# Optimization experiments

Measured on AMD Instinct MI355X. Metric: run time of the kernel, lower is better.

The kernel has to match this reference:

```python
import jax, jax.numpy as jnp
import numpy as np

B, C_IN, L = 4, 512, 16384
C_RED = C_IN // 2  # q/k/v reduced channels = 256
BL = 64            # sliding-window block size
NEG = -jnp.inf


def setup_inputs() -> dict:
    key = jax.random.key(0)
    ks = jax.random.split(key, 8)
    x1 = jax.random.normal(ks[0], (B, C_IN, L), dtype=jnp.float32)
    x2 = jax.random.normal(ks[1], (B, C_IN, L), dtype=jnp.float32)
    mask = jnp.ones((B, 1, L), dtype=jnp.float32)
    s = 0.02
    Wq = jax.random.normal(ks[2], (C_RED, C_IN), dtype=jnp.float32) * s
    Wk = jax.random.normal(ks[3], (C_RED, C_IN), dtype=jnp.float32) * s
    Wv = jax.random.normal(ks[4], (C_RED, C_IN), dtype=jnp.float32) * s
    Wo = jax.random.normal(ks[5], (C_IN, C_RED), dtype=jnp.float32) * s
    bq = jnp.zeros((C_RED,), jnp.float32)
    bk = jnp.zeros((C_RED,), jnp.float32)
    bv = jnp.zeros((C_RED,), jnp.float32)
    bo = jnp.zeros((C_IN,), jnp.float32)
    return {"x1": x1, "x2": x2, "mask": mask, "Wq": Wq, "bq": bq,
            "Wk": Wk, "bk": bk, "Wv": Wv, "bv": bv, "Wo": Wo, "bo": bo}


def _conv1x1(W, b, x):
    # x: (B, Cin, L) -> (B, Cout, L)
    return jnp.einsum('oc,bcl->bol', W, x) + b[None, :, None]


def reference(x1, x2, mask, Wq, bq, Wk, bk, Wv, bv, Wo, bo):
    # encoder stage: value comes from x1 (x2 unused)
    q = _conv1x1(Wq, bq, x1)  # (B, C, L)
    k = _conv1x1(Wk, bk, x1)
    v = _conv1x1(Wv, bv, x1)

    Bq, C, Lq = q.shape
    bl = BL
    nb = (Lq + bl - 1) // bl
    pad = nb * bl - Lq
    if pad > 0:
        q = jnp.pad(q, ((0, 0), (0, 0), (0, pad)))
        k = jnp.pad(k, ((0, 0), (0, 0), (0, pad)))
        v = jnp.pad(v, ((0, 0), (0, 0), (0, pad)))
        mask = jnp.pad(mask, ((0, 0), (0, 0), (0, pad)))

    # non-overlapping windows: (B, C, nb, bl)
    qb = q.reshape(Bq, C, nb, bl)
    kb = k.reshape(Bq, C, nb, bl)
    vb = v.reshape(Bq, C, nb, bl)
    mb = mask.reshape(Bq, 1, nb, bl)  # (B,1,nb,bl)

    scale = 1.0 / jnp.sqrt(jnp.float32(C))
    # per-block attention scores: (B, nb, bl_i, bl_j)
    scores = jnp.einsum('bcni,bcnj->bnij', qb, kb) * scale
    key_mask = mb[:, 0, :, None, :]  # (B, nb, 1, bl_j)
    scores = jnp.where(key_mask == 0, NEG, scores)
    probs = jax.nn.softmax(scores, axis=-1)
    attn = jnp.einsum('bnij,bcnj->bcni', probs, vb)  # (B, C, nb, bl)

    h = jax.nn.relu(attn)
    out = jnp.einsum('oc,bcni->boni', Wo, h) + bo[None, :, None, None]
    out = out.reshape(Bq, Wo.shape[0], nb * bl)
    if pad > 0:
        out = out[:, :, :Lq]
    return out
```

## Files before the change

### kernel.cpp

```cpp
#include <hip/hip_runtime.h>
#include <hip/hip_fp16.h>
#include <stdint.h>

#define BB    4
#define CIN   512
#define CRED  256
#define LL    16384
#define NBLK  256
#define WELEM 131072

typedef _Float16 half8 __attribute__((ext_vector_type(8)));
typedef float    f32x4 __attribute__((ext_vector_type(4)));

#define SWZ(r) (((r)&7)<<4)

#define QBASE   524288
#define TILE_E  16384
#define MAT_E   16777216
#define WS_NEED ((size_t)(QBASE + 3 * MAT_E) * 2)

__global__ void convert_weights(const float* __restrict__ Wq,
                                const float* __restrict__ Wk,
                                const float* __restrict__ Wv,
                                const float* __restrict__ Wo,
                                _Float16* __restrict__ dst) {
    int i = blockIdx.x * blockDim.x + threadIdx.x;
    int m = i >> 17;
    int e = i & (WELEM - 1);
    const float* src = (m == 0) ? Wq : (m == 1) ? Wk : (m == 2) ? Wv : Wo;
    dst[(size_t)m * WELEM + e] = (_Float16)src[e];
}

__global__ __launch_bounds__(256, 2)
void qkv_gemm(const float* __restrict__ x1, const _Float16* __restrict__ W,
              const float* __restrict__ bq, const float* __restrict__ bk,
              const float* __restrict__ bv, _Float16* __restrict__ ws) {
    extern __shared__ char lds[];
    const int tid = threadIdx.x;
    const int wid = tid >> 6;
    const int l15 = tid & 15;
    const int l4  = (tid & 63) >> 4;
    const int b   = blockIdx.x >> 8;
    const int n   = blockIdx.x & 255;

    {
        const int jx = tid & 15;
        const int rg = tid >> 4;
        const float* xp = x1 + ((size_t)b * CIN + 8 * rg) * LL + n * 64 + 4 * jx;
        #pragma unroll
        for (int i = 0; i < 4; ++i) {
            f32x4 r[8];
            #pragma unroll
            for (int r8 = 0; r8 < 8; ++r8)
                r[r8] = *(const f32x4*)(xp + (size_t)(128 * i + r8) * LL);
            #pragma unroll
            for (int u = 0; u < 4; ++u) {
                const int j = 4 * jx + u;
                union { _Float16 h[8]; half8 v; } pk;
                #pragma unroll
                for (int r8 = 0; r8 < 8; ++r8) pk.h[r8] = (_Float16)r[r8][u];
                *(half8*)(lds + j * 1024 + ((16 * rg + 256 * i) ^ SWZ(j))) = pk.v;
            }
        }
    }
    __syncthreads();

    const size_t t = (size_t)blockIdx.x * TILE_E;
    #pragma unroll
    for (int p = 0; p < 3; ++p) {
        f32x4 am[4][4];
        #pragma unroll
        for (int m = 0; m < 4; ++m)
            #pragma unroll
            for (int q = 0; q < 4; ++q) am[m][q] = (f32x4){0.f, 0.f, 0.f, 0.f};
        const _Float16* wp = W + (size_t)p * WELEM + (size_t)(wid * 64 + l15) * CIN + l4 * 8;
        #pragma unroll 4
        for (int ks = 0; ks < 16; ++ks) {
            const int kb = ks * 64 + l4 * 16;
            half8 xb[4];
            #pragma unroll
            for (int nt = 0; nt < 4; ++nt) {
                const int j = nt * 16 + l15;
                xb[nt] = *(const half8*)(lds + j * 1024 + (kb ^ SWZ(j)));
            }
            #pragma unroll
            for (int mt = 0; mt < 4; ++mt) {
                half8 wf = *(const half8*)(wp + mt * 16 * CIN + ks * 32);
                #pragma unroll
                for (int nt = 0; nt < 4; ++nt)
                    am[mt][nt] = __builtin_amdgcn_mfma_f32_16x16x32_f16(wf, xb[nt], am[mt][nt], 0, 0, 0);
            }
        }
        const float* bias = (p == 0) ? bq : (p == 1) ? bk : bv;
        if (p < 2) {
            _Float16* dst = ws + QBASE + (size_t)p * MAT_E + t;
            #pragma unroll
            for (int mt = 0; mt < 4; ++mt) {
                const int c0 = wid * 64 + mt * 16 + l4 * 4;
                f32x4 b4 = *(const f32x4*)(bias + c0);
                #pragma unroll
                for (int nt = 0; nt < 4; ++nt) {
                    const int j = nt * 16 + l15;
                    union { _Float16 h[4]; uint64_t q; } pk;
                    #pragma unroll
                    for (int ri = 0; ri < 4; ++ri)
                        pk.h[ri] = (_Float16)(am[mt][nt][ri] + b4[ri]);
                    *(uint64_t*)(dst + (size_t)j * 256 + c0) = pk.q;
                }
            }
        } else {
            _Float16* dst = ws + QBASE + 2 * (size_t)MAT_E + t;
            #pragma unroll
            for (int mt = 0; mt < 4; ++mt) {
                const int c0 = wid * 64 + mt * 16 + l4 * 4;
                f32x4 b4 = *(const f32x4*)(bias + c0);
                #pragma unroll
                for (int nt = 0; nt < 4; ++nt) {
                    const int j = nt * 16 + l15;
                    #pragma unroll
                    for (int ri = 0; ri < 4; ++ri)
                        dst[(size_t)(c0 + ri) * 64 + j] = (_Float16)(am[mt][nt][ri] + b4[ri]);
                }
            }
        }
    }
}

#define BH_OFF 0
#define BP_OFF 32768
#define LDS_B  40960

__global__ __launch_bounds__(256, 3)
void attn_out(const float* __restrict__ mask, const _Float16* __restrict__ ws,
              const float* __restrict__ bo, float* __restrict__ out) {
    extern __shared__ char lds[];
    const int tid = threadIdx.x;
    const int wid = tid >> 6;
    const int l15 = tid & 15;
    const int l4  = (tid & 63) >> 4;
    const int b   = blockIdx.x >> 8;
    const int n   = blockIdx.x & 255;

    const size_t t = (size_t)blockIdx.x * TILE_E;
    const _Float16* qt = ws + QBASE + t;
    const _Float16* kt = qt + MAT_E;
    const _Float16* vt = qt + 2 * (size_t)MAT_E;
    const _Float16* Wo = ws + 3 * (size_t)WELEM;

    {
        const int i0 = wid * 16;
        f32x4 sa[4];
        #pragma unroll
        for (int jt = 0; jt < 4; ++jt) sa[jt] = (f32x4){0.f, 0.f, 0.f, 0.f};
        #pragma unroll
        for (int ks = 0; ks < 8; ++ks) {
            half8 qa = *(const half8*)(qt + (size_t)(i0 + l15) * 256 + ks * 32 + l4 * 8);
            #pragma unroll
            for (int jt = 0; jt < 4; ++jt) {
                half8 kf = *(const half8*)(kt + (size_t)(jt * 16 + l15) * 256 + ks * 32 + l4 * 8);
                sa[jt] = __builtin_amdgcn_mfma_f32_16x16x32_f16(qa, kf, sa[jt], 0, 0, 0);
            }
        }
        float msk[4];
        #pragma unroll
        for (int jt = 0; jt < 4; ++jt)
            msk[jt] = mask[(size_t)b * LL + n * 64 + jt * 16 + l15];
        #pragma unroll
        for (int ri = 0; ri < 4; ++ri) {
            float v[4];
            #pragma unroll
            for (int jt = 0; jt < 4; ++jt)
                v[jt] = (msk[jt] == 0.f) ? -1e30f : sa[jt][ri] * 0.0625f;
            float mx = fmaxf(fmaxf(v[0], v[1]), fmaxf(v[2], v[3]));
            mx = fmaxf(mx, __shfl_xor(mx, 1));
            mx = fmaxf(mx, __shfl_xor(mx, 2));
            mx = fmaxf(mx, __shfl_xor(mx, 4));
            mx = fmaxf(mx, __shfl_xor(mx, 8));
            float e[4], sum = 0.f;
            #pragma unroll
            for (int jt = 0; jt < 4; ++jt) { e[jt] = __expf(v[jt] - mx); sum += e[jt]; }
            sum += __shfl_xor(sum, 1);
            sum += __shfl_xor(sum, 2);
            sum += __shfl_xor(sum, 4);
            sum += __shfl_xor(sum, 8);
            const float inv = 1.f / sum;
            const int i = i0 + l4 * 4 + ri;
            #pragma unroll
            for (int jt = 0; jt < 4; ++jt) {
                const int j = jt * 16 + l15;
                *(_Float16*)(lds + BP_OFF + i * 128 + ((2 * j) ^ SWZ(i))) =
                    (_Float16)(e[jt] * inv);
            }
        }
    }
    __syncthreads();

    {
        const int cb = wid * 64;
        f32x4 pv[4][4];
        #pragma unroll
        for (int m = 0; m < 4; ++m)
            #pragma unroll
            for (int q = 0; q < 4; ++q) pv[m][q] = (f32x4){0.f, 0.f, 0.f, 0.f};
        #pragma unroll
        for (int ks = 0; ks < 2; ++ks) {
            const int kb = ks * 64 + l4 * 16;
            half8 pb[4];
            #pragma unroll
            for (int nt = 0; nt < 4; ++nt) {
                const int i = nt * 16 + l15;
                pb[nt] = *(const half8*)(lds + BP_OFF + i * 128 + (kb ^ SWZ(i)));
            }
            #pragma unroll
            for (int mt = 0; mt < 4; ++mt) {
                half8 va = *(const half8*)(vt + (size_t)(cb + mt * 16 + l15) * 64 + ks * 32 + l4 * 8);
                #pragma unroll
                for (int nt = 0; nt < 4; ++nt)
                    pv[mt][nt] = __builtin_amdgcn_mfma_f32_16x16x32_f16(va, pb[nt], pv[mt][nt], 0, 0, 0);
            }
        }
        #pragma unroll
        for (int mt = 0; mt < 4; ++mt) {
            const int c0 = cb + mt * 16 + l4 * 4;
            #pragma unroll
            for (int nt = 0; nt < 4; ++nt) {
                const int j = nt * 16 + l15;
                union { _Float16 h[4]; uint64_t q; } hp;
                #pragma unroll
                for (int ri = 0; ri < 4; ++ri)
                    hp.h[ri] = (_Float16)fmaxf(pv[mt][nt][ri], 0.f);
                *(uint64_t*)(lds + BH_OFF + j * 512 + ((2 * c0) ^ SWZ(j))) = hp.q;
            }
        }
    }
    __syncthreads();

    #pragma unroll
    for (int op = 0; op < 2; ++op) {
        const int mbo = wid * 128 + op * 64;
        const _Float16* wob = Wo + (size_t)(mbo + l15) * CRED + l4 * 8;
        f32x4 oa[4][4];
        #pragma unroll
        for (int m = 0; m < 4; ++m)
            #pragma unroll
            for (int q = 0; q < 4; ++q) oa[m][q] = (f32x4){0.f, 0.f, 0.f, 0.f};
        #pragma unroll 4
        for (int ks = 0; ks < 8; ++ks) {
            const int kb = ks * 64 + l4 * 16;
            half8 hb[4];
            #pragma unroll
            for (int nt = 0; nt < 4; ++nt) {
                const int i = nt * 16 + l15;
                hb[nt] = *(const half8*)(lds + BH_OFF + i * 512 + (kb ^ SWZ(i)));
            }
            #pragma unroll
            for (int mt = 0; mt < 4; ++mt) {
                half8 wa = *(const half8*)(wob + mt * 16 * CRED + ks * 32);
                #pragma unroll
                for (int nt = 0; nt < 4; ++nt)
                    oa[mt][nt] = __builtin_amdgcn_mfma_f32_16x16x32_f16(wa, hb[nt], oa[mt][nt], 0, 0, 0);
            }
        }
        #pragma unroll
        for (int mt = 0; mt < 4; ++mt) {
            const int o0 = mbo + mt * 16 + l4 * 4;
            f32x4 bov = *(const f32x4*)(bo + o0);
            #pragma unroll
            for (int ri = 0; ri < 4; ++ri) {
                float* orow = out + ((size_t)b * CIN + (o0 + ri)) * LL + n * 64;
                #pragma unroll
                for (int nt = 0; nt < 4; ++nt)
                    orow[nt * 16 + l15] = oa[mt][nt][ri] + bov[ri];
            }
        }
    }
}

#define XT_OFF 0
#define Q_OFF  0
#define K_OFF  32768
#define V_OFF  32768
#define H_OFF  0
#define P_OFF  65536
#define MSK_OFF 73728
#define LDS_BYTES 73984

__global__ __launch_bounds__(256, 2)
void att_fused(const float* __restrict__ x1, const float* __restrict__ mask,
               const _Float16* __restrict__ W,
               const float* __restrict__ bq, const float* __restrict__ bk,
               const float* __restrict__ bv, const float* __restrict__ bo,
               float* __restrict__ out) {
    extern __shared__ char lds[];
    const int tid  = threadIdx.x;
    const int wid  = tid >> 6;
    const int lane = tid & 63;
    const int l15  = lane & 15;
    const int l4   = lane >> 4;
    const int blk  = blockIdx.x;
    const int b    = blk >> 8;
    const int n    = blk & 255;

    const _Float16* Wq = W;
    const _Float16* Wk = W + WELEM;
    const _Float16* Wv = W + 2 * WELEM;
    const _Float16* Wo = W + 3 * WELEM;

    {
        const int jx = tid & 15;
        const int rb = tid >> 4;
        const float* xbase = x1 + ((size_t)b * CIN + 2 * rb) * LL + n * 64 + 4 * jx;
        #pragma unroll
        for (int i = 0; i < 16; ++i) {
            f32x4 a = *(const f32x4*)(xbase + (size_t)(32 * i) * LL);
            f32x4 c = *(const f32x4*)(xbase + (size_t)(32 * i + 1) * LL);
            const int col = 4 * rb + 64 * i;
            #pragma unroll
            for (int u = 0; u < 4; ++u) {
                union { _Float16 h[2]; uint32_t w; } p;
                p.h[0] = (_Float16)a[u];
                p.h[1] = (_Float16)c[u];
                const int j = 4 * jx + u;
                *(uint32_t*)(lds + XT_OFF + j * 1024 + (col ^ SWZ(j))) = p.w;
            }
        }
        if (tid < 64)
            *(float*)(lds + MSK_OFF + tid * 4) = mask[(size_t)b * LL + n * 64 + tid];
    }
    __syncthreads();

    uint64_t qh[4][4], kh[4][4], vh[4][4];
    #pragma unroll
    for (int pass = 0; pass < 4; ++pass) {
        f32x4 aQ[4], aK[4], aV[4];
        #pragma unroll
        for (int q = 0; q < 4; ++q) {
            aQ[q] = (f32x4){0.f, 0.f, 0.f, 0.f};
            aK[q] = (f32x4){0.f, 0.f, 0.f, 0.f};
            aV[q] = (f32x4){0.f, 0.f, 0.f, 0.f};
        }
        const int mrow = wid * 64 + pass * 16 + l15;
        const _Float16* wqp = Wq + (size_t)mrow * CIN + l4 * 8;
        const _Float16* wkp = Wk + (size_t)mrow * CIN + l4 * 8;
        const _Float16* wvp = Wv + (size_t)mrow * CIN + l4 * 8;
        #pragma unroll 4
        for (int ks = 0; ks < 16; ++ks) {
            const int kb = ks * 64 + l4 * 16;
            half8 xb[4];
            #pragma unroll
            for (int nt = 0; nt < 4; ++nt) {
                const int j = nt * 16 + l15;
                xb[nt] = *(const half8*)(lds + XT_OFF + j * 1024 + (kb ^ SWZ(j)));
            }
            half8 aq = *(const half8*)(wqp + ks * 32);
            half8 ak = *(const half8*)(wkp + ks * 32);
            half8 av = *(const half8*)(wvp + ks * 32);
            #pragma unroll
            for (int nt = 0; nt < 4; ++nt) {
                aQ[nt] = __builtin_amdgcn_mfma_f32_16x16x32_f16(aq, xb[nt], aQ[nt], 0, 0, 0);
                aK[nt] = __builtin_amdgcn_mfma_f32_16x16x32_f16(ak, xb[nt], aK[nt], 0, 0, 0);
                aV[nt] = __builtin_amdgcn_mfma_f32_16x16x32_f16(av, xb[nt], aV[nt], 0, 0, 0);
            }
        }
        const int c0 = wid * 64 + pass * 16 + l4 * 4;
        f32x4 bqv = *(const f32x4*)(bq + c0);
        f32x4 bkv = *(const f32x4*)(bk + c0);
        f32x4 bvv = *(const f32x4*)(bv + c0);
        #pragma unroll
        for (int nt = 0; nt < 4; ++nt) {
            union { _Float16 h[4]; uint64_t q; } qp, kp, vp;
            #pragma unroll
            for (int ri = 0; ri < 4; ++ri) {
                qp.h[ri] = (_Float16)(aQ[nt][ri] + bqv[ri]);
                kp.h[ri] = (_Float16)(aK[nt][ri] + bkv[ri]);
                vp.h[ri] = (_Float16)(aV[nt][ri] + bvv[ri]);
            }
            qh[pass][nt] = qp.q;
            kh[pass][nt] = kp.q;
            vh[pass][nt] = vp.q;
        }
    }
    __syncthreads();

    #pragma unroll
    for (int pass = 0; pass < 4; ++pass) {
        const int c0 = wid * 64 + pass * 16 + l4 * 4;
        #pragma unroll
        for (int nt = 0; nt < 4; ++nt) {
            const int j = nt * 16 + l15;
            *(uint64_t*)(lds + Q_OFF + j * 512 + ((2 * c0) ^ SWZ(j))) = qh[pass][nt];
            *(uint64_t*)(lds + K_OFF + j * 512 + ((2 * c0) ^ SWZ(j))) = kh[pass][nt];
        }
    }
    __syncthreads();

    {
        const int i0 = wid * 16;
        f32x4 sa[4];
        #pragma unroll
        for (int jt = 0; jt < 4; ++jt) sa[jt] = (f32x4){0.f, 0.f, 0.f, 0.f};
        #pragma unroll
        for (int ks = 0; ks < 8; ++ks) {
            const int kb = ks * 64 + l4 * 16;
            const int iq = i0 + l15;
            half8 qa = *(const half8*)(lds + Q_OFF + iq * 512 + (kb ^ SWZ(iq)));
            #pragma unroll
            for (int jt = 0; jt < 4; ++jt) {
                const int jr = jt * 16 + l15;
                half8 kf = *(const half8*)(lds + K_OFF + jr * 512 + (kb ^ SWZ(jr)));
                sa[jt] = __builtin_amdgcn_mfma_f32_16x16x32_f16(qa, kf, sa[jt], 0, 0, 0);
            }
        }
        float msk[4];
        #pragma unroll
        for (int jt = 0; jt < 4; ++jt)
            msk[jt] = *(const float*)(lds + MSK_OFF + (jt * 16 + l15) * 4);
        #pragma unroll
        for (int ri = 0; ri < 4; ++ri) {
            float v[4];
            #pragma unroll
            for (int jt = 0; jt < 4; ++jt)
                v[jt] = (msk[jt] == 0.f) ? -1e30f : sa[jt][ri] * 0.0625f;
            float mx = fmaxf(fmaxf(v[0], v[1]), fmaxf(v[2], v[3]));
            mx = fmaxf(mx, __shfl_xor(mx, 1));
            mx = fmaxf(mx, __shfl_xor(mx, 2));
            mx = fmaxf(mx, __shfl_xor(mx, 4));
            mx = fmaxf(mx, __shfl_xor(mx, 8));
            float e[4], sum = 0.f;
            #pragma unroll
            for (int jt = 0; jt < 4; ++jt) { e[jt] = __expf(v[jt] - mx); sum += e[jt]; }
            sum += __shfl_xor(sum, 1);
            sum += __shfl_xor(sum, 2);
            sum += __shfl_xor(sum, 4);
            sum += __shfl_xor(sum, 8);
            const float inv = 1.f / sum;
            const int i = i0 + l4 * 4 + ri;
            #pragma unroll
            for (int jt = 0; jt < 4; ++jt) {
                const int j = jt * 16 + l15;
                *(_Float16*)(lds + P_OFF + i * 128 + ((2 * j) ^ SWZ(i))) =
                    (_Float16)(e[jt] * inv);
            }
        }
    }
    __syncthreads();

    #pragma unroll
    for (int pass = 0; pass < 4; ++pass) {
        const int c0 = wid * 64 + pass * 16 + l4 * 4;
        #pragma unroll
        for (int nt = 0; nt < 4; ++nt) {
            const int j = nt * 16 + l15;
            const uint64_t v64 = vh[pass][nt];
            #pragma unroll
            for (int ri = 0; ri < 4; ++ri) {
                const int c = c0 + ri;
                *(uint16_t*)(lds + V_OFF + c * 128 + ((2 * j) ^ SWZ(c))) =
                    (uint16_t)(v64 >> (16 * ri));
            }
        }
    }
    __syncthreads();

    {
        const int cb = wid * 64;
        f32x4 pv[4][4];
        #pragma unroll
        for (int m = 0; m < 4; ++m)
            #pragma unroll
            for (int q = 0; q < 4; ++q) pv[m][q] = (f32x4){0.f, 0.f, 0.f, 0.f};
        #pragma unroll
        for (int ks = 0; ks < 2; ++ks) {
            const int kb = ks * 64 + l4 * 16;
            half8 pb[4];
            #pragma unroll
            for (int nt = 0; nt < 4; ++nt) {
                const int i = nt * 16 + l15;
                pb[nt] = *(const half8*)(lds + P_OFF + i * 128 + (kb ^ SWZ(i)));
            }
            #pragma unroll
            for (int mt = 0; mt < 4; ++mt) {
                const int c = cb + mt * 16 + l15;
                half8 va = *(const half8*)(lds + V_OFF + c * 128 + ((kb) ^ SWZ(c)));
                #pragma unroll
                for (int nt = 0; nt < 4; ++nt)
                    pv[mt][nt] = __builtin_amdgcn_mfma_f32_16x16x32_f16(va, pb[nt], pv[mt][nt], 0, 0, 0);
            }
        }
        #pragma unroll
        for (int mt = 0; mt < 4; ++mt) {
            const int c0 = cb + mt * 16 + l4 * 4;
            #pragma unroll
            for (int nt = 0; nt < 4; ++nt) {
                const int j = nt * 16 + l15;
                union { _Float16 h[4]; uint64_t q; } hp;
                #pragma unroll
                for (int ri = 0; ri < 4; ++ri)
                    hp.h[ri] = (_Float16)fmaxf(pv[mt][nt][ri], 0.f);
                *(uint64_t*)(lds + H_OFF + j * 512 + ((2 * c0) ^ SWZ(j))) = hp.q;
            }
        }
    }
    __syncthreads();

    #pragma unroll
    for (int op = 0; op < 2; ++op) {
        const int mbo = wid * 128 + op * 64;
        const _Float16* wob = Wo + (size_t)(mbo + l15) * CRED + l4 * 8;
        f32x4 oa[4][4];
        #pragma unroll
        for (int m = 0; m < 4; ++m)
            #pragma unroll
            for (int q = 0; q < 4; ++q) oa[m][q] = (f32x4){0.f, 0.f, 0.f, 0.f};
        #pragma unroll 4
        for (int ks = 0; ks < 8; ++ks) {
            const int kb = ks * 64 + l4 * 16;
            half8 hb[4];
            #pragma unroll
            for (int nt = 0; nt < 4; ++nt) {
                const int i = nt * 16 + l15;
                hb[nt] = *(const half8*)(lds + H_OFF + i * 512 + (kb ^ SWZ(i)));
            }
            #pragma unroll
            for (int mt = 0; mt < 4; ++mt) {
                half8 wa = *(const half8*)(wob + mt * 16 * CRED + ks * 32);
                #pragma unroll
                for (int nt = 0; nt < 4; ++nt)
                    oa[mt][nt] = __builtin_amdgcn_mfma_f32_16x16x32_f16(wa, hb[nt], oa[mt][nt], 0, 0, 0);
            }
        }
        #pragma unroll
        for (int mt = 0; mt < 4; ++mt) {
            const int o0 = mbo + mt * 16 + l4 * 4;
            f32x4 bov = *(const f32x4*)(bo + o0);
            #pragma unroll
            for (int ri = 0; ri < 4; ++ri) {
                float* orow = out + ((size_t)b * CIN + (o0 + ri)) * LL + n * 64;
                #pragma unroll
                for (int nt = 0; nt < 4; ++nt)
                    orow[nt * 16 + l15] = oa[mt][nt][ri] + bov[ri];
            }
        }
    }
}

extern "C" void kernel_launch(void* const* d_in, const int* in_sizes, int n_in,
                              void* d_out, int out_size, void* d_ws, size_t ws_size,
                              hipStream_t stream) {
    const float* x1   = (const float*)d_in[0];
    const float* mask = (const float*)d_in[2];
    const float* Wq   = (const float*)d_in[3];
    const float* bq   = (const float*)d_in[4];
    const float* Wk   = (const float*)d_in[5];
    const float* bk   = (const float*)d_in[6];
    const float* Wv   = (const float*)d_in[7];
    const float* bv   = (const float*)d_in[8];
    const float* Wo   = (const float*)d_in[9];
    const float* bo   = (const float*)d_in[10];
    float* out = (float*)d_out;
    _Float16* wbuf = (_Float16*)d_ws;

    convert_weights<<<2048, 256, 0, stream>>>(Wq, Wk, Wv, Wo, wbuf);

    if (ws_size >= WS_NEED) {
        (void)hipFuncSetAttribute((const void*)qkv_gemm,
                                  hipFuncAttributeMaxDynamicSharedMemorySize, 65536);
        qkv_gemm<<<BB * NBLK, 256, 65536, stream>>>(x1, wbuf, bq, bk, bv, wbuf);
        attn_out<<<BB * NBLK, 256, LDS_B, stream>>>(mask, wbuf, bo, out);
    } else {
        (void)hipFuncSetAttribute((const void*)att_fused,
                                  hipFuncAttributeMaxDynamicSharedMemorySize, LDS_BYTES);
        att_fused<<<BB * NBLK, 256, LDS_BYTES, stream>>>(x1, mask, wbuf, bq, bk, bv, bo, out);
    }
}
```

Baseline: 202.6 us.

## Double-buffer x1 loads in QKV GEMM with 128-position tiles and staged coalesced stores

The QKV projection kernel now handles 128 positions per block instead of 64, which halves the grid. It streams the 512 input channels in 64-channel chunks through a double-buffered LDS ring, so the global loads of x1 overlap with MFMA work instead of staging all of x1 up front. Outputs are transposed through LDS and written with coalesced 16-byte stores. V is now stored as a (B, C, L) channel-major global layout, and attn_out's addressing is updated to match. The change adds extra barriers per chunk and uses a larger accumulator array, 4x8 f32x4 per thread, which raises register pressure.

```diff
diff --git a/kernel.cpp b/kernel.cpp
--- a/kernel.cpp
+++ b/kernel.cpp
@@ -15,7 +15,6 @@
 #define SWZ(r) (((r)&7)<<4)
 
 #define QBASE   524288
-#define TILE_E  16384
 #define MAT_E   16777216
 #define WS_NEED ((size_t)(QBASE + 3 * MAT_E) * 2)
 
@@ -40,90 +39,150 @@
     const int wid = tid >> 6;
     const int l15 = tid & 15;
     const int l4  = (tid & 63) >> 4;
-    const int b   = blockIdx.x >> 8;
-    const int n   = blockIdx.x & 255;
-
-    {
-        const int jx = tid & 15;
-        const int rg = tid >> 4;
-        const float* xp = x1 + ((size_t)b * CIN + 8 * rg) * LL + n * 64 + 4 * jx;
-        #pragma unroll
-        for (int i = 0; i < 4; ++i) {
-            f32x4 r[8];
-            #pragma unroll
-            for (int r8 = 0; r8 < 8; ++r8)
-                r[r8] = *(const f32x4*)(xp + (size_t)(128 * i + r8) * LL);
-            #pragma unroll
-            for (int u = 0; u < 4; ++u) {
-                const int j = 4 * jx + u;
-                union { _Float16 h[8]; half8 v; } pk;
-                #pragma unroll
-                for (int r8 = 0; r8 < 8; ++r8) pk.h[r8] = (_Float16)r[r8][u];
-                *(half8*)(lds + j * 1024 + ((16 * rg + 256 * i) ^ SWZ(j))) = pk.v;
-            }
-        }
-    }
-    __syncthreads();
-
-    const size_t t = (size_t)blockIdx.x * TILE_E;
+    const int b   = blockIdx.x >> 7;
+    const int g   = blockIdx.x & 127;
+    const int pos0 = g * 128;
+
+    const int jx = tid & 31;
+    const int rg = tid >> 5;
+
+    const float* xb0 = x1 + (size_t)b * CIN * LL + pos0 + 4 * jx;
+
+    f32x4 st[8];
+
+    #define X_ISSUE(KC) do {                                                  \
+        const float* xp_ = xb0 + (size_t)((KC) * 64 + 8 * rg) * LL;           \
+        _Pragma("unroll")                                                     \
+        for (int r8_ = 0; r8_ < 8; ++r8_)                                     \
+            st[r8_] = *(const f32x4*)(xp_ + (size_t)r8_ * LL);                \
+    } while (0)
+
+    #define X_COMMIT(CUR) do {                                                \
+        char* bp_ = lds + (CUR) * 16384;                                      \
+        _Pragma("unroll")                                                     \
+        for (int u_ = 0; u_ < 4; ++u_) {                                      \
+            const int n_ = 4 * jx + u_;                                       \
+            union { _Float16 h[8]; half8 v; } pk_;                            \
+            _Pragma("unroll")                                                 \
+            for (int r8_ = 0; r8_ < 8; ++r8_)                                 \
+                pk_.h[r8_] = (_Float16)st[r8_][u_];                           \
+            *(half8*)(bp_ + n_ * 128 + ((16 * rg) ^ SWZ(n_))) = pk_.v;        \
+        }                                                                     \
+    } while (0)
+
+    X_ISSUE(0);
+    X_COMMIT(0);
+    __syncthreads();
+    int cur = 0;
+
     #pragma unroll
     for (int p = 0; p < 3; ++p) {
-        f32x4 am[4][4];
-        #pragma unroll
-        for (int m = 0; m < 4; ++m)
-            #pragma unroll
-            for (int q = 0; q < 4; ++q) am[m][q] = (f32x4){0.f, 0.f, 0.f, 0.f};
-        const _Float16* wp = W + (size_t)p * WELEM + (size_t)(wid * 64 + l15) * CIN + l4 * 8;
-        #pragma unroll 4
-        for (int ks = 0; ks < 16; ++ks) {
-            const int kb = ks * 64 + l4 * 16;
-            half8 xb[4];
-            #pragma unroll
-            for (int nt = 0; nt < 4; ++nt) {
-                const int j = nt * 16 + l15;
-                xb[nt] = *(const half8*)(lds + j * 1024 + (kb ^ SWZ(j)));
-            }
-            #pragma unroll
-            for (int mt = 0; mt < 4; ++mt) {
-                half8 wf = *(const half8*)(wp + mt * 16 * CIN + ks * 32);
-                #pragma unroll
-                for (int nt = 0; nt < 4; ++nt)
-                    am[mt][nt] = __builtin_amdgcn_mfma_f32_16x16x32_f16(wf, xb[nt], am[mt][nt], 0, 0, 0);
-            }
-        }
-        const float* bias = (p == 0) ? bq : (p == 1) ? bk : bv;
+        f32x4 acc[4][8];
+        #pragma unroll
+        for (int mt = 0; mt < 4; ++mt)
+            #pragma unroll
+            for (int nt = 0; nt < 8; ++nt) acc[mt][nt] = (f32x4){0.f, 0.f, 0.f, 0.f};
+
+        for (int kc = 0; kc < 8; ++kc) {
+            const bool hn = !(p == 2 && kc == 7);
+            if (hn) X_ISSUE((kc + 1) & 7);
+
+            const _Float16* wp = W + (size_t)p * WELEM
+                               + (size_t)(wid * 64 + l15) * CIN + kc * 64 + l4 * 8;
+            char* bp = lds + cur * 16384;
+            #pragma unroll
+            for (int ks = 0; ks < 2; ++ks) {
+                half8 xf[8];
+                #pragma unroll
+                for (int nt = 0; nt < 8; ++nt) {
+                    const int n = nt * 16 + l15;
+                    xf[nt] = *(const half8*)(bp + n * 128 + ((ks * 64 + l4 * 16) ^ SWZ(n)));
+                }
+                #pragma unroll
+                for (int mt = 0; mt < 4; ++mt) {
+                    half8 wf = *(const half8*)(wp + mt * 16 * CIN + ks * 32);
+                    #pragma unroll
+                    for (int nt = 0; nt < 8; ++nt)
+                        acc[mt][nt] = __builtin_amdgcn_mfma_f32_16x16x32_f16(wf, xf[nt], acc[mt][nt], 0, 0, 0);
+                }
+            }
+            __syncthreads();
+            if (hn) X_COMMIT(cur ^ 1);
+            cur ^= 1;
+            __syncthreads();
+        }
+
+        char* rp = lds + 32768;
         if (p < 2) {
-            _Float16* dst = ws + QBASE + (size_t)p * MAT_E + t;
-            #pragma unroll
-            for (int mt = 0; mt < 4; ++mt) {
-                const int c0 = wid * 64 + mt * 16 + l4 * 4;
-                f32x4 b4 = *(const f32x4*)(bias + c0);
-                #pragma unroll
-                for (int nt = 0; nt < 4; ++nt) {
-                    const int j = nt * 16 + l15;
-                    union { _Float16 h[4]; uint64_t q; } pk;
+            _Float16* qdst = ws + QBASE + (size_t)p * MAT_E
+                           + ((size_t)b * LL + pos0) * CRED;
+            const float* bias = p ? bk : bq;
+            #pragma unroll
+            for (int r = 0; r < 2; ++r) {
+                #pragma unroll
+                for (int mt = 0; mt < 4; ++mt) {
+                    const int c0 = wid * 64 + mt * 16 + l4 * 4;
+                    f32x4 bb = *(const f32x4*)(bias + c0);
                     #pragma unroll
-                    for (int ri = 0; ri < 4; ++ri)
-                        pk.h[ri] = (_Float16)(am[mt][nt][ri] + b4[ri]);
-                    *(uint64_t*)(dst + (size_t)j * 256 + c0) = pk.q;
+                    for (int q4 = 0; q4 < 4; ++q4) {
+                        const int nt = 4 * r + q4;
+                        const int nn = (nt * 16 + l15) - 64 * r;
+                        union { _Float16 h[4]; uint64_t q; } pk;
+                        #pragma unroll
+                        for (int ri = 0; ri < 4; ++ri)
+                            pk.h[ri] = (_Float16)(acc[mt][nt][ri] + bb[ri]);
+                        *(uint64_t*)(rp + nn * 512 + ((2 * c0) ^ SWZ(nn))) = pk.q;
+                    }
                 }
+                __syncthreads();
+                #pragma unroll
+                for (int i = 0; i < 8; ++i) {
+                    const int chunk = i * 4096 + tid * 16;
+                    const int nn = chunk >> 9;
+                    const int mc = chunk & 511;
+                    half8 v = *(const half8*)(rp + nn * 512 + (mc ^ SWZ(nn)));
+                    *(half8*)((char*)qdst + (size_t)(64 * r + nn) * 512 + mc) = v;
+                }
+                __syncthreads();
             }
         } else {
-            _Float16* dst = ws + QBASE + 2 * (size_t)MAT_E + t;
-            #pragma unroll
-            for (int mt = 0; mt < 4; ++mt) {
-                const int c0 = wid * 64 + mt * 16 + l4 * 4;
-                f32x4 b4 = *(const f32x4*)(bias + c0);
-                #pragma unroll
-                for (int nt = 0; nt < 4; ++nt) {
-                    const int j = nt * 16 + l15;
+            _Float16* vdst = ws + QBASE + 2 * (size_t)MAT_E
+                           + (size_t)b * CRED * LL + pos0;
+            #pragma unroll
+            for (int r = 0; r < 2; ++r) {
+                if ((wid >> 1) == r) {
+                    const int mw = (wid & 1) * 64;
                     #pragma unroll
-                    for (int ri = 0; ri < 4; ++ri)
-                        dst[(size_t)(c0 + ri) * 64 + j] = (_Float16)(am[mt][nt][ri] + b4[ri]);
+                    for (int mt = 0; mt < 4; ++mt) {
+                        const int c0 = wid * 64 + mt * 16 + l4 * 4;
+                        f32x4 bb = *(const f32x4*)(bv + c0);
+                        #pragma unroll
+                        for (int nt = 0; nt < 8; ++nt) {
+                            const int n = nt * 16 + l15;
+                            #pragma unroll
+                            for (int ri = 0; ri < 4; ++ri) {
+                                const int m = mw + mt * 16 + l4 * 4 + ri;
+                                *(_Float16*)(rp + m * 256 + ((2 * n) ^ SWZ(m))) =
+                                    (_Float16)(acc[mt][nt][ri] + bb[ri]);
+                            }
+                        }
+                    }
                 }
-            }
-        }
-    }
+                __syncthreads();
+                #pragma unroll
+                for (int i = 0; i < 8; ++i) {
+                    const int chunk = i * 4096 + tid * 16;
+                    const int m  = chunk >> 8;
+                    const int nc = chunk & 255;
+                    half8 v = *(const half8*)(rp + m * 256 + (nc ^ SWZ(m)));
+                    *(half8*)((char*)vdst + (size_t)(128 * r + m) * (size_t)(LL * 2) + nc) = v;
+                }
+                __syncthreads();
+            }
+        }
+    }
+    #undef X_ISSUE
+    #undef X_COMMIT
 }
 
 #define BH_OFF 0
@@ -141,10 +200,9 @@
     const int b   = blockIdx.x >> 8;
     const int n   = blockIdx.x & 255;
 
-    const size_t t = (size_t)blockIdx.x * TILE_E;
-    const _Float16* qt = ws + QBASE + t;
+    const _Float16* qt = ws + QBASE + ((size_t)b * LL + n * 64) * CRED;
     const _Float16* kt = qt + MAT_E;
-    const _Float16* vt = qt + 2 * (size_t)MAT_E;
+    const _Float16* vt = ws + QBASE + 2 * (size_t)MAT_E + (size_t)b * CRED * LL + n * 64;
     const _Float16* Wo = ws + 3 * (size_t)WELEM;
 
     {
@@ -154,10 +212,10 @@
         for (int jt = 0; jt < 4; ++jt) sa[jt] = (f32x4){0.f, 0.f, 0.f, 0.f};
         #pragma unroll
         for (int ks = 0; ks < 8; ++ks) {
-            half8 qa = *(const half8*)(qt + (size_t)(i0 + l15) * 256 + ks * 32 + l4 * 8);
+            half8 qa = *(const half8*)(qt + (size_t)(i0 + l15) * CRED + ks * 32 + l4 * 8);
             #pragma unroll
             for (int jt = 0; jt < 4; ++jt) {
-                half8 kf = *(const half8*)(kt + (size_t)(jt * 16 + l15) * 256 + ks * 32 + l4 * 8);
+                half8 kf = *(const half8*)(kt + (size_t)(jt * 16 + l15) * CRED + ks * 32 + l4 * 8);
                 sa[jt] = __builtin_amdgcn_mfma_f32_16x16x32_f16(qa, kf, sa[jt], 0, 0, 0);
             }
         }
@@ -213,7 +271,7 @@
             }
             #pragma unroll
             for (int mt = 0; mt < 4; ++mt) {
-                half8 va = *(const half8*)(vt + (size_t)(cb + mt * 16 + l15) * 64 + ks * 32 + l4 * 8);
+                half8 va = *(const half8*)(vt + (size_t)(cb + mt * 16 + l15) * LL + ks * 32 + l4 * 8);
                 #pragma unroll
                 for (int nt = 0; nt < 4; ++nt)
                     pv[mt][nt] = __builtin_amdgcn_mfma_f32_16x16x32_f16(va, pb[nt], pv[mt][nt], 0, 0, 0);
@@ -481,7 +539,7 @@
             #pragma unroll
             for (int mt = 0; mt < 4; ++mt) {
                 const int c = cb + mt * 16 + l15;
-                half8 va = *(const half8*)(lds + V_OFF + c * 128 + ((kb) ^ SWZ(c)));
+                half8 va = *(const half8*)(lds + V_OFF + c * 128 + (kb ^ SWZ(c)));
                 #pragma unroll
                 for (int nt = 0; nt < 4; ++nt)
                     pv[mt][nt] = __builtin_amdgcn_mfma_f32_16x16x32_f16(va, pb[nt], pv[mt][nt], 0, 0, 0);
@@ -565,7 +623,7 @@
     if (ws_size >= WS_NEED) {
         (void)hipFuncSetAttribute((const void*)qkv_gemm,
                                   hipFuncAttributeMaxDynamicSharedMemorySize, 65536);
-        qkv_gemm<<<BB * NBLK, 256, 65536, stream>>>(x1, wbuf, bq, bk, bv, wbuf);
+        qkv_gemm<<<BB * 128, 256, 65536, stream>>>(x1, wbuf, bq, bk, bv, wbuf);
         attn_out<<<BB * NBLK, 256, LDS_B, stream>>>(mask, wbuf, bo, out);
     } else {
         (void)hipFuncSetAttribute((const void*)att_fused,
```

After: 187.1 us. -7.7%, faster.

## Double-buffer QKV GEMM fragments, hoist x loads, change V workspace layout

Applied to the files above, without the earlier changes.

The QKV projection kernel now issues all global loads of the x tile before converting them, and double-buffers the weight and LDS fragments so the next k-step's loads overlap the current MFMAs. The V workspace layout changes from per-tile contiguous (c,64) blocks to a global (b, c, L) layout with stride LL, and attn_out is updated to match. This is meant to hide load latency in the GEMM, at the cost of more registers, which could hurt occupancy under launch_bounds(256,2). The V layout change also makes V reads and writes strided across rows.

```diff
diff --git a/kernel.cpp b/kernel.cpp
--- a/kernel.cpp
+++ b/kernel.cpp
@@ -15,7 +15,6 @@
 #define SWZ(r) (((r)&7)<<4)
 
 #define QBASE   524288
-#define TILE_E  16384
 #define MAT_E   16777216
 #define WS_NEED ((size_t)(QBASE + 3 * MAT_E) * 2)
 
@@ -47,79 +46,101 @@
         const int jx = tid & 15;
         const int rg = tid >> 4;
         const float* xp = x1 + ((size_t)b * CIN + 8 * rg) * LL + n * 64 + 4 * jx;
+        f32x4 st[4][8];
+        #pragma unroll
+        for (int i = 0; i < 4; ++i)
+            #pragma unroll
+            for (int r8 = 0; r8 < 8; ++r8)
+                st[i][r8] = *(const f32x4*)(xp + (size_t)(128 * i + r8) * LL);
+        asm volatile("" ::: "memory");
         #pragma unroll
         for (int i = 0; i < 4; ++i) {
-            f32x4 r[8];
-            #pragma unroll
-            for (int r8 = 0; r8 < 8; ++r8)
-                r[r8] = *(const f32x4*)(xp + (size_t)(128 * i + r8) * LL);
             #pragma unroll
             for (int u = 0; u < 4; ++u) {
                 const int j = 4 * jx + u;
                 union { _Float16 h[8]; half8 v; } pk;
                 #pragma unroll
-                for (int r8 = 0; r8 < 8; ++r8) pk.h[r8] = (_Float16)r[r8][u];
+                for (int r8 = 0; r8 < 8; ++r8) pk.h[r8] = (_Float16)st[i][r8][u];
                 *(half8*)(lds + j * 1024 + ((16 * rg + 256 * i) ^ SWZ(j))) = pk.v;
             }
         }
     }
     __syncthreads();
 
-    const size_t t = (size_t)blockIdx.x * TILE_E;
     #pragma unroll
     for (int p = 0; p < 3; ++p) {
-        f32x4 am[4][4];
-        #pragma unroll
-        for (int m = 0; m < 4; ++m)
-            #pragma unroll
-            for (int q = 0; q < 4; ++q) am[m][q] = (f32x4){0.f, 0.f, 0.f, 0.f};
-        const _Float16* wp = W + (size_t)p * WELEM + (size_t)(wid * 64 + l15) * CIN + l4 * 8;
-        #pragma unroll 4
+        f32x4 acc[4][4];
+        #pragma unroll
+        for (int mt = 0; mt < 4; ++mt)
+            #pragma unroll
+            for (int q = 0; q < 4; ++q) acc[mt][q] = (f32x4){0.f, 0.f, 0.f, 0.f};
+
+        const _Float16* wp = W + (size_t)p * WELEM
+                           + (size_t)(wid * 64 + l15) * CIN + l4 * 8;
+
+        half8 wf[2][4], xf[2][4];
+        #pragma unroll
+        for (int mt = 0; mt < 4; ++mt) wf[0][mt] = *(const half8*)(wp + mt * 16 * CIN);
+        #pragma unroll
+        for (int nt = 0; nt < 4; ++nt) {
+            const int j = nt * 16 + l15;
+            xf[0][nt] = *(const half8*)(lds + j * 1024 + ((l4 * 16) ^ SWZ(j)));
+        }
+
+        #pragma unroll
         for (int ks = 0; ks < 16; ++ks) {
-            const int kb = ks * 64 + l4 * 16;
-            half8 xb[4];
-            #pragma unroll
-            for (int nt = 0; nt < 4; ++nt) {
-                const int j = nt * 16 + l15;
-                xb[nt] = *(const half8*)(lds + j * 1024 + (kb ^ SWZ(j)));
-            }
-            #pragma unroll
-            for (int mt = 0; mt < 4; ++mt) {
-                half8 wf = *(const half8*)(wp + mt * 16 * CIN + ks * 32);
-                #pragma unroll
-                for (int nt = 0; nt < 4; ++nt)
-                    am[mt][nt] = __builtin_amdgcn_mfma_f32_16x16x32_f16(wf, xb[nt], am[mt][nt], 0, 0, 0);
-            }
-        }
-        const float* bias = (p == 0) ? bq : (p == 1) ? bk : bv;
+            const int c = ks & 1, nx = c ^ 1;
+            if (ks < 15) {
+                const int kb = (ks + 1) * 64 + l4 * 16;
+                #pragma unroll
+                for (int mt = 0; mt < 4; ++mt)
+                    wf[nx][mt] = *(const half8*)(wp + mt * 16 * CIN + (ks + 1) * 32);
+                #pragma unroll
+                for (int nt = 0; nt < 4; ++nt) {
+                    const int j = nt * 16 + l15;
+                    xf[nx][nt] = *(const half8*)(lds + j * 1024 + (kb ^ SWZ(j)));
+                }
+            }
+            #pragma unroll
+            for (int mt = 0; mt < 4; ++mt)
+                #pragma unroll
+                for (int nt = 0; nt < 4; ++nt)
+                    acc[mt][nt] = __builtin_amdgcn_mfma_f32_16x16x32_f16(
+                        wf[c][mt], xf[c][nt], acc[mt][nt], 0, 0, 0);
+        }
+
         if (p < 2) {
-            _Float16* dst = ws + QBASE + (size_t)p * MAT_E + t;
+            _Float16* dst = ws + QBASE + (size_t)p * MAT_E
+                          + ((size_t)b * LL + n * 64) * CRED;
+            const float* bias = p ? bk : bq;
             #pragma unroll
             for (int mt = 0; mt < 4; ++mt) {
                 const int c0 = wid * 64 + mt * 16 + l4 * 4;
                 f32x4 b4 = *(const f32x4*)(bias + c0);
                 #pragma unroll
                 for (int nt = 0; nt < 4; ++nt) {
-                    const int j = nt * 16 + l15;
+                    const int pos = nt * 16 + l15;
                     union { _Float16 h[4]; uint64_t q; } pk;
                     #pragma unroll
                     for (int ri = 0; ri < 4; ++ri)
-                        pk.h[ri] = (_Float16)(am[mt][nt][ri] + b4[ri]);
-                    *(uint64_t*)(dst + (size_t)j * 256 + c0) = pk.q;
+                        pk.h[ri] = (_Float16)(acc[mt][nt][ri] + b4[ri]);
+                    *(uint64_t*)(dst + (size_t)pos * CRED + c0) = pk.q;
                 }
             }
         } else {
-            _Float16* dst = ws + QBASE + 2 * (size_t)MAT_E + t;
+            _Float16* vdst = ws + QBASE + 2 * (size_t)MAT_E
+                           + (size_t)b * CRED * LL + n * 64;
             #pragma unroll
             for (int mt = 0; mt < 4; ++mt) {
                 const int c0 = wid * 64 + mt * 16 + l4 * 4;
-                f32x4 b4 = *(const f32x4*)(bias + c0);
+                f32x4 b4 = *(const f32x4*)(bv + c0);
                 #pragma unroll
                 for (int nt = 0; nt < 4; ++nt) {
-                    const int j = nt * 16 + l15;
+                    const int pos = nt * 16 + l15;
                     #pragma unroll
                     for (int ri = 0; ri < 4; ++ri)
-                        dst[(size_t)(c0 + ri) * 64 + j] = (_Float16)(am[mt][nt][ri] + b4[ri]);
+                        vdst[(size_t)(c0 + ri) * LL + pos] =
+                            (_Float16)(acc[mt][nt][ri] + b4[ri]);
                 }
             }
         }
@@ -141,10 +162,9 @@
     const int b   = blockIdx.x >> 8;
     const int n   = blockIdx.x & 255;
 
-    const size_t t = (size_t)blockIdx.x * TILE_E;
-    const _Float16* qt = ws + QBASE + t;
+    const _Float16* qt = ws + QBASE + ((size_t)b * LL + n * 64) * CRED;
     const _Float16* kt = qt + MAT_E;
-    const _Float16* vt = qt + 2 * (size_t)MAT_E;
+    const _Float16* vt = ws + QBASE + 2 * (size_t)MAT_E + (size_t)b * CRED * LL + n * 64;
     const _Float16* Wo = ws + 3 * (size_t)WELEM;
 
     {
@@ -154,10 +174,10 @@
         for (int jt = 0; jt < 4; ++jt) sa[jt] = (f32x4){0.f, 0.f, 0.f, 0.f};
         #pragma unroll
         for (int ks = 0; ks < 8; ++ks) {
-            half8 qa = *(const half8*)(qt + (size_t)(i0 + l15) * 256 + ks * 32 + l4 * 8);
+            half8 qa = *(const half8*)(qt + (size_t)(i0 + l15) * CRED + ks * 32 + l4 * 8);
             #pragma unroll
             for (int jt = 0; jt < 4; ++jt) {
-                half8 kf = *(const half8*)(kt + (size_t)(jt * 16 + l15) * 256 + ks * 32 + l4 * 8);
+                half8 kf = *(const half8*)(kt + (size_t)(jt * 16 + l15) * CRED + ks * 32 + l4 * 8);
                 sa[jt] = __builtin_amdgcn_mfma_f32_16x16x32_f16(qa, kf, sa[jt], 0, 0, 0);
             }
         }
@@ -213,7 +233,7 @@
             }
             #pragma unroll
             for (int mt = 0; mt < 4; ++mt) {
-                half8 va = *(const half8*)(vt + (size_t)(cb + mt * 16 + l15) * 64 + ks * 32 + l4 * 8);
+                half8 va = *(const half8*)(vt + (size_t)(cb + mt * 16 + l15) * LL + ks * 32 + l4 * 8);
                 #pragma unroll
                 for (int nt = 0; nt < 4; ++nt)
                     pv[mt][nt] = __builtin_amdgcn_mfma_f32_16x16x32_f16(va, pb[nt], pv[mt][nt], 0, 0, 0);
@@ -481,7 +501,7 @@
             #pragma unroll
             for (int mt = 0; mt < 4; ++mt) {
                 const int c = cb + mt * 16 + l15;
-                half8 va = *(const half8*)(lds + V_OFF + c * 128 + ((kb) ^ SWZ(c)));
+                half8 va = *(const half8*)(lds + V_OFF + c * 128 + (kb ^ SWZ(c)));
                 #pragma unroll
                 for (int nt = 0; nt < 4; ++nt)
                     pv[mt][nt] = __builtin_amdgcn_mfma_f32_16x16x32_f16(va, pb[nt], pv[mt][nt], 0, 0, 0);
```

New measurement: 199.0 us. About the same (-1.8%).
